# Optimization experiments

Measured on AMD Instinct MI355X. Metric: run time of the kernel, lower is better.

Reference implementation:

```python
import jax, jax.numpy as jnp
import numpy as np

B, FI, FO, K, DIM_STYLE, H, W = 8, 512, 512, 3, 512, 64, 64
EPS = 1e-8


def setup_inputs() -> dict:
    key = jax.random.key(0)
    ks = jax.random.split(key, 5)
    return {
        "x": jax.random.normal(ks[0], (B, FI, H, W), dtype=jnp.float32),
        "style": jax.random.normal(ks[1], (B, DIM_STYLE), dtype=jnp.float32),
        "w": jax.random.normal(ks[2], (FO, FI, K, K), dtype=jnp.float32),
        "mod_w": jax.random.normal(ks[3], (FI, DIM_STYLE), dtype=jnp.float32),
        "mod_b": jax.random.normal(ks[4], (FI,), dtype=jnp.float32),
    }


def _fir_filter(dtype):
    # upfirdn2d.setup_filter([1,3,3,1]): normalize 1D to sum 1, outer product -> 4x4, sum 1
    f1 = jnp.array([1.0, 3.0, 3.0, 1.0], dtype=dtype)
    f1 = f1 / jnp.sum(f1)
    f = jnp.outer(f1, f1)
    # gain = up**2 = 4 applied inside upfirdn2d; filter is symmetric so flip is a no-op
    return (f * 4.0)[::-1, ::-1]


def _mod_conv_up(x, style, w, mod_w, mod_b):
    # modLinear: F.linear(style, mod_w * dim_style**-0.5, bias=mod_b)
    s = style @ (mod_w * (DIM_STYLE ** -0.5)).T + mod_b  # [B, FI]
    # modulate: w_scale * style broadcast over input channels
    w_scale = (FI * K * K) ** -0.5
    wm = w[None] * (w_scale * s[:, None, :, None, None])  # [B, FO, FI, K, K]
    # demodulate
    demod = jax.lax.rsqrt(jnp.sum(wm * wm, axis=(2, 3, 4)) + EPS)  # [B, FO]
    wm = wm * demod[:, :, None, None, None]
    # conv2d_resample up=2 fast path == conv_transpose2d(stride=2, padding=0) per sample,
    def tconv(xs, ws):  # xs [FI,H,W], ws [FO,FI,K,K]
        y = jax.lax.conv_general_dilated(
            xs[None], ws[:, :, ::-1, ::-1],
            window_strides=(1, 1), padding=[(K - 1, K - 1), (K - 1, K - 1)],
            lhs_dilation=(2, 2),
            dimension_numbers=("NCHW", "OIHW", "NCHW"))
        return y[0]

    y = jax.vmap(tconv)(x, wm)  # [B, FO, 2H+1, 2W+1]
    # FIR low-pass: upfirdn2d(pad=[1,1,1,1], gain=4) -> output [B, FO, 2H, 2W]
    f = _fir_filter(y.dtype)
    Bn, C, Hh, Ww = y.shape
    yf = y.reshape(Bn * C, 1, Hh, Ww)
    yf = jax.lax.conv_general_dilated(
        yf, f[None, None], window_strides=(1, 1), padding=[(1, 1), (1, 1)],
        dimension_numbers=("NCHW", "OIHW", "NCHW"))
    return yf.reshape(Bn, C, Hh - 1, Ww - 1)


def reference(x, style, w, mod_w, mod_b):
    return _mod_conv_up(x, style, w, mod_w, mod_b)
```

## Files before the change

kernel.cpp:

```cpp
#include <hip/hip_runtime.h>

typedef _Float16 f16;
typedef f16 f16x8 __attribute__((ext_vector_type(8)));
typedef float f32x4 __attribute__((ext_vector_type(4)));

#define OFF_SMOD  0u
#define OFF_SSQ   16384u
#define OFF_DEMOD 32768u
#define OFF_WSQ   49152u
#define OFF_WPAR  1097728u
#define OFF_XP    5816320u
#define XP_BYTES  35685376u
#define OFF_YP    41501696u
#define PLANE     4560

__global__ void style_kernel(const float* __restrict__ style, const float* __restrict__ mod_w,
                             const float* __restrict__ mod_b, float* __restrict__ smod,
                             float* __restrict__ ssq) {
    int b = blockIdx.x;
    int fi = threadIdx.x;
    __shared__ float st[512];
    st[fi] = style[b * 512 + fi];
    __syncthreads();
    float sum = 0.f;
    const float* mw = mod_w + (size_t)fi * 512;
    for (int d = 0; d < 512; ++d) sum += st[d] * mw[d];
    float s = sum * 0.04419417382415922f  + mod_b[fi];
    smod[b * 512 + fi] = s * 0.014731391274719741f ;
    ssq[b * 512 + fi] = s * s;
}

__global__ void wsq_kernel(const float* __restrict__ w, float* __restrict__ wsq) {
    int fo = blockIdx.x;
    int fi = threadIdx.x;
    const float* p = w + ((size_t)fo * 512 + fi) * 9;
    float s = 0.f;
#pragma unroll
    for (int k = 0; k < 9; ++k) { float v = p[k]; s += v * v; }
    wsq[fo * 512 + fi] = s;
}

__global__ void demod_kernel(const float* __restrict__ ssq, const float* __restrict__ wsq,
                             float* __restrict__ demod) {
    int b = blockIdx.x >> 1;
    int fo = (blockIdx.x & 1) * 256 + threadIdx.x;
    __shared__ float sq[512];
    for (int i = threadIdx.x; i < 512; i += 256) sq[i] = ssq[b * 512 + i];
    __syncthreads();
    float sum = 0.f;
    const float* wr = wsq + (size_t)fo * 512;
    for (int fi = 0; fi < 512; ++fi) sum += sq[fi] * wr[fi];
    demod[b * 512 + fo] = rsqrtf(sum * (1.0f / 4608.0f) + 1e-8f);
}

__global__ void xp_kernel(const float* __restrict__ x, const float* __restrict__ smod,
                          f16* __restrict__ xp) {
    int id = blockIdx.x;
    int fc = id & 7;
    int h = (id >> 3) & 63;
    int b = id >> 9;
    int fi0 = fc * 64;
    __shared__ f16 tile[64 * 65];
    int tid = threadIdx.x;
#pragma unroll
    for (int it = 0; it < 16; ++it) {
        int e = it * 256 + tid;
        int i = e >> 6, wc = e & 63;
        float v = x[(((size_t)(b * 512 + fi0 + i)) * 64 + h) * 64 + wc];
        tile[i * 65 + wc] = (f16)(v * smod[b * 512 + fi0 + i]);
    }
    __syncthreads();
#pragma unroll
    for (int it = 0; it < 16; ++it) {
        int e = it * 256 + tid;
        int wc = e >> 6, i = e & 63;
        xp[((size_t)(b * 4356 + (h + 1) * 66 + (wc + 1))) * 512 + fi0 + i] = tile[i * 65 + wc];
    }
}

__global__ void wpar2_kernel(const float* __restrict__ w, f16* __restrict__ wpar2) {
    const int wi_[9] = {8, 6, 2, 0, 7, 1, 5, 3, 4};
    int fo = blockIdx.x;
#pragma unroll
    for (int half = 0; half < 2; ++half) {
        int fi = half * 256 + threadIdx.x;
        const float* p = w + ((size_t)fo * 512 + fi) * 9;
        int fc = fi >> 5, ch = fi & 31;
#pragma unroll
        for (int s = 0; s < 9; ++s)
            wpar2[(((size_t)s * 16 + fc) * 512 + fo) * 32 + ch] = (f16)p[wi_[s]];
    }
}

__global__ void ring2_kernel(f16* __restrict__ P) {
    int idx = blockIdx.x * 256 + threadIdx.x;
    if (idx >= 16384 * 133) return;
    int slab = idx / 133, r = idx - slab * 133;
    f16* base = P + (size_t)slab * PLANE;
    if (r < 68) base[r] = (f16)0.f;
    else base[(r - 67) * 68] = (f16)0.f;
}

template <int C>
__device__ __forceinline__ void tconv3_body(const f16* __restrict__ wpar2, const f16* __restrict__ xp,
                                            f16* __restrict__ P, f16* Xs, int b, int fo0, int n0, int h) {
    constexpr int NT = (C == 0) ? 4 : (C == 3) ? 1 : 2;
    constexpr int LNT = (C == 0) ? 2 : (C == 3) ? 0 : 1;
    constexpr int SB = (C == 0) ? 0 : (C == 1) ? 4 : (C == 2) ? 6 : 8;
    constexpr int DELT[4] = {(C == 0) ? 0 : (C == 1) ? 1 : (C == 2) ? 66 : 67,
                             (C == 0) ? 1 : 67, 66, 67};
    constexpr int Q = 16 * NT;

    int tid = threadIdx.x, lane = tid & 63;
    int kb = lane >> 4, lr = lane & 15;
    int wbase = b * 4356 + n0;
    int rmax = 4356 - n0;

    f32x4 acc[4][4];
#pragma unroll
    for (int m = 0; m < 4; ++m)
#pragma unroll
        for (int n = 0; n < 4; ++n) acc[m][n] = (f32x4){0.f, 0.f, 0.f, 0.f};

    int4 xr[2];
    f16x8 afr[3][4], bfr[2][4];

    int u1 = tid, r1 = u1 >> 2, p1 = u1 & 3;
    bool has2 = tid < 12;
    int u2 = tid + 512, r2 = u2 >> 2, p2 = u2 & 3;
    const f16* xrow1 = xp + (size_t)(wbase + r1) * 512 + p1 * 8;
    const f16* xrow2 = xp + (size_t)(wbase + r2) * 512 + p2 * 8;
    char* wdst1 = (char*)Xs + ((u1 ^ (r1 & 7)) << 4);
    char* wdst2 = (char*)Xs + ((u2 ^ (r2 & 7)) << 4);
    bool v1 = r1 <= rmax;
    bool v2 = has2 && (r2 <= rmax);

    auto loadX = [&](int k) {
        int off = k * 32;
        int4 a = {0, 0, 0, 0}, c2 = {0, 0, 0, 0};
        if (v1) a = *(const int4*)(xrow1 + off);
        if (v2) c2 = *(const int4*)(xrow2 + off);
        xr[0] = a; xr[1] = c2;
    };
    auto writeX = [&](int buf) {
        *(int4*)(wdst1 + buf * 8448) = xr[0];
        if (has2) *(int4*)(wdst2 + buf * 8448) = xr[1];
    };
    auto loadA = [&](int q, f16x8* dst) {
        int sl = SB + (q & (NT - 1));
        int kk = q >> LNT;
        const f16* p = wpar2 + ((size_t)(sl * 16 + kk) * 512 + fo0 + h * 64 + lr) * 32 + kb * 8;
#pragma unroll
        for (int m = 0; m < 4; ++m) dst[m] = *(const f16x8*)(p + m * 16 * 32);
    };
    auto readBF = [&](int buf, int delt, f16x8* dst) {
#pragma unroll
        for (int nf = 0; nf < 4; ++nf) {
            int rr = nf * 16 + lr + delt;
            dst[nf] = *(const f16x8*)((const char*)Xs + buf * 8448 + (((rr * 4 + kb) ^ (rr & 7)) << 4));
        }
    };

    loadX(0);
    writeX(0);
    loadX(1);
    loadA(0, afr[0]);
    loadA(1, afr[1]);

#pragma unroll 6
    for (int k = 0; k < 16; ++k) {
        if (k < 15) {
            writeX((k + 1) % 3);
            if (k < 14) loadX(k + 2);
            asm volatile("s_waitcnt lgkmcnt(0)\n\ts_barrier" ::: "memory");
        }
        const int cur = k % 3;
        readBF(cur, DELT[0], bfr[(k * NT) & 1]);
#pragma unroll
        for (int tap = 0; tap < NT; ++tap) {
            const int q = k * NT + tap;
            if (q + 2 < Q) loadA(q + 2, afr[(q + 2) % 3]);
            if (tap + 1 < NT) {
                readBF(cur, DELT[tap + 1], bfr[(q + 1) & 1]);
            }
            __builtin_amdgcn_s_setprio(1);
#pragma unroll
            for (int m = 0; m < 4; ++m)
#pragma unroll
                for (int nf = 0; nf < 4; ++nf)
                    acc[m][nf] = __builtin_amdgcn_mfma_f32_16x16x32_f16(afr[q % 3][m], bfr[q & 1][nf], acc[m][nf], 0, 0, 0);
            __builtin_amdgcn_s_setprio(0);
            if (tap + 1 == NT && k < 15) {
            }
        }
    }

    size_t slab = (size_t)(C * 8 + b) * 512;
#pragma unroll
    for (int m = 0; m < 4; ++m) {
#pragma unroll
        for (int j = 0; j < 4; ++j) {
            int fo = fo0 + h * 64 + m * 16 + kb * 4 + j;
            f16* pb = P + (slab + fo) * PLANE;
#pragma unroll
            for (int nf = 0; nf < 4; ++nf) {
                int nn = n0 + nf * 16 + lr;
                int t = (nn * 993) >> 16;
                int s = nn - t * 66;
                pb[(t + 1) * 68 + (s + 1)] = (f16)acc[m][nf][j];
            }
        }
    }
}

__global__ __launch_bounds__(512, 2) void tconv3_kernel(const f16* __restrict__ wpar2,
                                                        const f16* __restrict__ xp,
                                                        f16* __restrict__ P) {
    __shared__ __align__(16) f16 Xs[3 * 528 * 8];
    int id = blockIdx.x;
    int g = id & 7;
    int fg = g >> 1;
    int bh = g & 1;
    int rest = id >> 3;
    int bq = rest / 68;
    int n0t = rest - bq * 68;
    int b = bh * 4 + bq;
    int fo0 = fg << 7, n0 = n0t << 6;
    int w = threadIdx.x >> 6;
    int h = w >> 2;
    int c = (w == 0 || w == 5) ? 0 : (w == 2 || w == 7) ? 1 : (w == 3 || w == 6) ? 2 : 3;
    switch (c) {
        case 0: tconv3_body<0>(wpar2, xp, P, Xs, b, fo0, n0, h); break;
        case 1: tconv3_body<1>(wpar2, xp, P, Xs, b, fo0, n0, h); break;
        case 2: tconv3_body<2>(wpar2, xp, P, Xs, b, fo0, n0, h); break;
        default: tconv3_body<3>(wpar2, xp, P, Xs, b, fo0, n0, h); break;
    }
}

__global__ __launch_bounds__(256, 4) void fir3_kernel(const f16* __restrict__ P,
                                                      const float* __restrict__ demod,
                                                      float* __restrict__ out) {
    int bid = blockIdx.x;
    int b = bid & 7, fo = bid >> 3;
    __shared__ __align__(16) f16 yr[4][4488];
    const size_t pstep = (size_t)8 * 512 * PLANE;
    int tid = threadIdx.x;
    const f16* src0 = P + ((size_t)(b * 512 + fo)) * PLANE;
#pragma unroll
    for (int c = 0; c < 4; ++c) {
        const int4* src = (const int4*)(src0 + c * pstep);
        int4* dst = (int4*)(&yr[c][0]);
#pragma unroll
        for (int it = 0; it < 3; ++it) {
            int idx = it * 256 + tid;
            if (idx < 561) dst[idx] = src[idx];
        }
    }
    __syncthreads();
    float dm = demod[b * 512 + fo];
    int OX = tid & 127, rg = tid >> 7;
    int OYb = rg * 64;
    int e = OX & 1;
    int c0o = (1 - e) * 4488 + (((OX - 1) >> 1) + 1);
    int c1o = e * 4488 + ((OX >> 1) + 1);
    int c2o = (1 - e) * 4488 + (((OX + 1) >> 1) + 1);
    int c3o = e * 4488 + (((OX + 2) >> 1) + 1);
    const f16* yf = &yr[0][0];
    size_t obase = ((size_t)(b * 512 + fo)) * 16384 + OX;
    float h0 = 0.f, h1 = 0.f, h2 = 0.f, h3 = 0.f;
#pragma unroll 4
    for (int i = 0; i < 67; ++i) {
        int oy = OYb - 1 + i;
        int base = (oy & 1) * (2 * 4488) + ((oy >> 1) + 1) * 68;
        float h = 0.25f * ((float)yf[base + c0o] + (float)yf[base + c3o])
                + 0.75f * ((float)yf[base + c1o] + (float)yf[base + c2o]);
        h0 = h1; h1 = h2; h2 = h3; h3 = h;
        if (i >= 3) {
            float a = 0.25f * (h0 + h3) + 0.75f * (h1 + h2);
            out[obase + (size_t)(OYb + i - 3) * 128] = a * dm;
        }
    }
}

extern "C" void kernel_launch(void* const* d_in, const int* in_sizes, int n_in,
                              void* d_out, int out_size, void* d_ws, size_t ws_size,
                              hipStream_t stream) {
    const float* x = (const float*)d_in[0];
    const float* style = (const float*)d_in[1];
    const float* w = (const float*)d_in[2];
    const float* mod_w = (const float*)d_in[3];
    const float* mod_b = (const float*)d_in[4];
    float* out = (float*)d_out;

    char* ws = (char*)d_ws;
    float* smod = (float*)(ws + OFF_SMOD);
    float* ssq = (float*)(ws + OFF_SSQ);
    float* demod = (float*)(ws + OFF_DEMOD);
    float* wsq = (float*)(ws + OFF_WSQ);
    f16* wpar2 = (f16*)(ws + OFF_WPAR);
    f16* xp = (f16*)(ws + OFF_XP);
    f16* P = (f16*)(ws + OFF_YP);

    style_kernel<<<8, 512, 0, stream>>>(style, mod_w, mod_b, smod, ssq);
    wsq_kernel<<<512, 512, 0, stream>>>(w, wsq);
    demod_kernel<<<16, 256, 0, stream>>>(ssq, wsq, demod);
    wpar2_kernel<<<512, 256, 0, stream>>>(w, wpar2);
    hipMemsetAsync(xp, 0, XP_BYTES, stream);
    xp_kernel<<<4096, 256, 0, stream>>>(x, smod, xp);
    ring2_kernel<<<8512, 256, 0, stream>>>(P);
    tconv3_kernel<<<2176, 512, 0, stream>>>(wpar2, xp, P);
    fir3_kernel<<<4096, 256, 0, stream>>>(P, demod, out);
}
```

Measured before the change: 434.5 us.

## Double the spatial tile of the transposed-conv GEMM to 128 columns

The tconv kernel now computes 128 output positions per block instead of 64, so each wave holds a 4x8 accumulator grid and reuses every weight fragment across twice as many MFMAs. Grid size halves to 1088 blocks. The LDS pipeline for the input tile drops from triple to double buffering with a larger 784-row buffer, and weight prefetch depth drops from two stages to one. This cuts repeated weight loads from global memory per output, but raises register pressure, shortens the prefetch distance, and leaves fewer blocks for load balancing across CUs.

```diff
diff --git a/kernel.cpp b/kernel.cpp
--- a/kernel.cpp
+++ b/kernel.cpp
@@ -102,7 +102,7 @@
 }
 
 template <int C>
-__device__ __forceinline__ void tconv3_body(const f16* __restrict__ wpar2, const f16* __restrict__ xp,
+__device__ __forceinline__ void tconv4_body(const f16* __restrict__ wpar2, const f16* __restrict__ xp,
                                             f16* __restrict__ P, f16* Xs, int b, int fo0, int n0, int h) {
     constexpr int NT = (C == 0) ? 4 : (C == 3) ? 1 : 2;
     constexpr int LNT = (C == 0) ? 2 : (C == 3) ? 0 : 1;
@@ -110,28 +110,29 @@
     constexpr int DELT[4] = {(C == 0) ? 0 : (C == 1) ? 1 : (C == 2) ? 66 : 67,
                              (C == 0) ? 1 : 67, 66, 67};
     constexpr int Q = 16 * NT;
+    constexpr int BUFB = 784 * 16;
 
     int tid = threadIdx.x, lane = tid & 63;
     int kb = lane >> 4, lr = lane & 15;
     int wbase = b * 4356 + n0;
     int rmax = 4356 - n0;
 
-    f32x4 acc[4][4];
+    f32x4 acc[4][8];
 #pragma unroll
     for (int m = 0; m < 4; ++m)
 #pragma unroll
-        for (int n = 0; n < 4; ++n) acc[m][n] = (f32x4){0.f, 0.f, 0.f, 0.f};
-
-    int4 xr[2];
-    f16x8 afr[3][4], bfr[2][4];
+        for (int n = 0; n < 8; ++n) acc[m][n] = (f32x4){0.f, 0.f, 0.f, 0.f};
+
+    int4 xr0, xr1;
+    f16x8 af[2][4], bfA[4], bfB[4];
 
     int u1 = tid, r1 = u1 >> 2, p1 = u1 & 3;
-    bool has2 = tid < 12;
+    bool has2 = tid < 268;
     int u2 = tid + 512, r2 = u2 >> 2, p2 = u2 & 3;
     const f16* xrow1 = xp + (size_t)(wbase + r1) * 512 + p1 * 8;
     const f16* xrow2 = xp + (size_t)(wbase + r2) * 512 + p2 * 8;
-    char* wdst1 = (char*)Xs + ((u1 ^ (r1 & 7)) << 4);
-    char* wdst2 = (char*)Xs + ((u2 ^ (r2 & 7)) << 4);
+    int wd1 = (u1 ^ (r1 & 7)) << 4;
+    int wd2 = (u2 ^ (r2 & 7)) << 4;
     bool v1 = r1 <= rmax;
     bool v2 = has2 && (r2 <= rmax);
 
@@ -140,11 +141,11 @@
         int4 a = {0, 0, 0, 0}, c2 = {0, 0, 0, 0};
         if (v1) a = *(const int4*)(xrow1 + off);
         if (v2) c2 = *(const int4*)(xrow2 + off);
-        xr[0] = a; xr[1] = c2;
+        xr0 = a; xr1 = c2;
     };
     auto writeX = [&](int buf) {
-        *(int4*)(wdst1 + buf * 8448) = xr[0];
-        if (has2) *(int4*)(wdst2 + buf * 8448) = xr[1];
+        *(int4*)((char*)Xs + buf * BUFB + wd1) = xr0;
+        if (has2) *(int4*)((char*)Xs + buf * BUFB + wd2) = xr1;
     };
     auto loadA = [&](int q, f16x8* dst) {
         int sl = SB + (q & (NT - 1));
@@ -153,45 +154,47 @@
 #pragma unroll
         for (int m = 0; m < 4; ++m) dst[m] = *(const f16x8*)(p + m * 16 * 32);
     };
-    auto readBF = [&](int buf, int delt, f16x8* dst) {
+    auto readBF = [&](int buf, int delt, int half, f16x8* dst) {
 #pragma unroll
         for (int nf = 0; nf < 4; ++nf) {
-            int rr = nf * 16 + lr + delt;
-            dst[nf] = *(const f16x8*)((const char*)Xs + buf * 8448 + (((rr * 4 + kb) ^ (rr & 7)) << 4));
+            int rr = (half * 4 + nf) * 16 + lr + delt;
+            int u = rr * 4 + kb;
+            dst[nf] = *(const f16x8*)((const char*)Xs + buf * BUFB + ((u ^ (rr & 7)) << 4));
         }
     };
 
     loadX(0);
     writeX(0);
     loadX(1);
-    loadA(0, afr[0]);
-    loadA(1, afr[1]);
-
-#pragma unroll 6
+    loadA(0, af[0]);
+
+#pragma unroll 2
     for (int k = 0; k < 16; ++k) {
-        if (k < 15) {
-            writeX((k + 1) % 3);
-            if (k < 14) loadX(k + 2);
-            asm volatile("s_waitcnt lgkmcnt(0)\n\ts_barrier" ::: "memory");
-        }
-        const int cur = k % 3;
-        readBF(cur, DELT[0], bfr[(k * NT) & 1]);
+        asm volatile("s_waitcnt lgkmcnt(0)\n\ts_barrier" ::: "memory");
+        if (k < 15) writeX((k + 1) & 1);
+        if (k < 14) loadX(k + 2);
+        const int cur = k & 1;
+        readBF(cur, DELT[0], 0, bfA);
 #pragma unroll
         for (int tap = 0; tap < NT; ++tap) {
             const int q = k * NT + tap;
-            if (q + 2 < Q) loadA(q + 2, afr[(q + 2) % 3]);
-            if (tap + 1 < NT) {
-                readBF(cur, DELT[tap + 1], bfr[(q + 1) & 1]);
-            }
+            if (q + 1 < Q) loadA(q + 1, af[(q + 1) & 1]);
+            readBF(cur, DELT[tap], 1, bfB);
             __builtin_amdgcn_s_setprio(1);
 #pragma unroll
             for (int m = 0; m < 4; ++m)
 #pragma unroll
                 for (int nf = 0; nf < 4; ++nf)
-                    acc[m][nf] = __builtin_amdgcn_mfma_f32_16x16x32_f16(afr[q % 3][m], bfr[q & 1][nf], acc[m][nf], 0, 0, 0);
+                    acc[m][nf] = __builtin_amdgcn_mfma_f32_16x16x32_f16(af[q & 1][m], bfA[nf], acc[m][nf], 0, 0, 0);
             __builtin_amdgcn_s_setprio(0);
-            if (tap + 1 == NT && k < 15) {
-            }
+            if (tap + 1 < NT) readBF(cur, DELT[tap + 1], 0, bfA);
+            __builtin_amdgcn_s_setprio(1);
+#pragma unroll
+            for (int m = 0; m < 4; ++m)
+#pragma unroll
+                for (int nf = 0; nf < 4; ++nf)
+                    acc[m][4 + nf] = __builtin_amdgcn_mfma_f32_16x16x32_f16(af[q & 1][m], bfB[nf], acc[m][4 + nf], 0, 0, 0);
+            __builtin_amdgcn_s_setprio(0);
         }
     }
 
@@ -203,7 +206,7 @@
             int fo = fo0 + h * 64 + m * 16 + kb * 4 + j;
             f16* pb = P + (slab + fo) * PLANE;
 #pragma unroll
-            for (int nf = 0; nf < 4; ++nf) {
+            for (int nf = 0; nf < 8; ++nf) {
                 int nn = n0 + nf * 16 + lr;
                 int t = (nn * 993) >> 16;
                 int s = nn - t * 66;
@@ -213,27 +216,27 @@
     }
 }
 
-__global__ __launch_bounds__(512, 2) void tconv3_kernel(const f16* __restrict__ wpar2,
+__global__ __launch_bounds__(512, 2) void tconv4_kernel(const f16* __restrict__ wpar2,
                                                         const f16* __restrict__ xp,
                                                         f16* __restrict__ P) {
-    __shared__ __align__(16) f16 Xs[3 * 528 * 8];
+    __shared__ __align__(16) f16 Xs[2 * 784 * 8];
     int id = blockIdx.x;
     int g = id & 7;
     int fg = g >> 1;
     int bh = g & 1;
     int rest = id >> 3;
-    int bq = rest / 68;
-    int n0t = rest - bq * 68;
+    int bq = rest / 34;
+    int n0t = rest - bq * 34;
     int b = bh * 4 + bq;
-    int fo0 = fg << 7, n0 = n0t << 6;
+    int fo0 = fg << 7, n0 = n0t << 7;
     int w = threadIdx.x >> 6;
     int h = w >> 2;
     int c = (w == 0 || w == 5) ? 0 : (w == 2 || w == 7) ? 1 : (w == 3 || w == 6) ? 2 : 3;
     switch (c) {
-        case 0: tconv3_body<0>(wpar2, xp, P, Xs, b, fo0, n0, h); break;
-        case 1: tconv3_body<1>(wpar2, xp, P, Xs, b, fo0, n0, h); break;
-        case 2: tconv3_body<2>(wpar2, xp, P, Xs, b, fo0, n0, h); break;
-        default: tconv3_body<3>(wpar2, xp, P, Xs, b, fo0, n0, h); break;
+        case 0: tconv4_body<0>(wpar2, xp, P, Xs, b, fo0, n0, h); break;
+        case 1: tconv4_body<1>(wpar2, xp, P, Xs, b, fo0, n0, h); break;
+        case 2: tconv4_body<2>(wpar2, xp, P, Xs, b, fo0, n0, h); break;
+        default: tconv4_body<3>(wpar2, xp, P, Xs, b, fo0, n0, h); break;
     }
 }
 
@@ -308,6 +311,6 @@
     hipMemsetAsync(xp, 0, XP_BYTES, stream);
     xp_kernel<<<4096, 256, 0, stream>>>(x, smod, xp);
     ring2_kernel<<<8512, 256, 0, stream>>>(P);
-    tconv3_kernel<<<2176, 512, 0, stream>>>(wpar2, xp, P);
+    tconv4_kernel<<<1088, 512, 0, stream>>>(wpar2, xp, P);
     fir3_kernel<<<4096, 256, 0, stream>>>(P, demod, out);
 }
```

After: 785.0 us. 80.7% more time.
